# Kernel optimization log

Hardware: AMD Instinct MI355X
Metric: run time of the kernel (lower is better)

The kernel has to match this reference:

```python
import jax, jax.numpy as jnp
import numpy as np

CUTOFF = 3.6
WIDTH = 0.3
N_MAX = 12
N_TYPES = 3
Y00 = 0.28209479177387814  # 1/sqrt(4*pi)
# GTO radial widths: sigma_n = cutoff * max(sqrt(n),1) / n_max
_SIGMA = np.array([CUTOFF * max(np.sqrt(n), 1.0) / N_MAX for n in range(N_MAX)], dtype=np.float32)
_NPOW = np.arange(N_MAX, dtype=np.float32)


def _cutoff_fn(r):
    # shifted cosine: 1 below cutoff-width, smooth cosine taper, 0 beyond cutoff
    start = CUTOFF - WIDTH
    taper = 0.5 * (1.0 + jnp.cos(jnp.pi * (r - start) / WIDTH))
    return jnp.where(r < start, 1.0, jnp.where(r < CUTOFF, taper, 0.0))


def _radial(r):
    # GTO-like basis: R_n(r) = r^n * exp(-r^2 / (2 sigma_n^2)), shape [E, N_MAX]
    r_ = r[:, None]
    return (r_ ** _NPOW) * jnp.exp(-0.5 * (r_ / _SIGMA) ** 2)


def _sph_harm(u):
    # real spherical harmonics up to l=2 on unit vectors u=[E,3] -> [E,9]
    x, y, z = u[:, 0], u[:, 1], u[:, 2]
    one = jnp.ones_like(x)
    return jnp.stack([
        0.28209479177387814 * one,                       # l=0
        0.4886025119029199 * y,                          # l=1, m=-1
        0.4886025119029199 * z,                          # l=1, m=0
        0.4886025119029199 * x,                          # l=1, m=+1
        1.0925484305920792 * x * y,                      # l=2, m=-2
        1.0925484305920792 * y * z,                      # l=2, m=-1
        0.31539156525252005 * (3.0 * z * z - 1.0),       # l=2, m=0
        1.0925484305920792 * x * z,                      # l=2, m=+1
        0.5462742152960396 * (x * x - y * y),            # l=2, m=+2
    ], axis=-1)


def _soap_energy(positions, weight, bias, atom_types, pairs):
    N = positions.shape[0]
    i, j = pairs[:, 0], pairs[:, 1]
    rij = positions[j] - positions[i]                     # [E,3] gather
    r = jnp.sqrt(jnp.sum(rij * rij, axis=-1) + 1e-12)     # [E]
    u = rij / r[:, None]
    # per-edge basis: [E, n, lm]
    B = _radial(r)[:, :, None] * _sph_harm(u)[:, None, :] * _cutoff_fn(r)[:, None, None]
    # scatter-sum by (center atom, neighbor species)
    seg = i.astype(jnp.int32) * N_TYPES + atom_types[j]
    c = jax.ops.segment_sum(B, seg, num_segments=N * N_TYPES)
    c = c.reshape(N, N_TYPES, N_MAX, 9)                    # [N, a, n, lm]
    # center-atom self density (r=0: only n=0, l=0 survives), weight 1.0
    c = c.at[jnp.arange(N), atom_types, 0, 0].add(Y00)
    # power spectrum per l block
    blocks = []
    for l, (lo, hi) in enumerate([(0, 1), (1, 4), (4, 9)]):
        cl = c[:, :, :, lo:hi]
        p = jnp.einsum('ianm,ibkm->ianbk', cl, cl) / jnp.sqrt(2.0 * l + 1.0)
        blocks.append(p)
    feats = jnp.stack(blocks, axis=-1).reshape(N, -1)      # [N, 3888]
    pooled = feats.sum(axis=0, keepdims=True)              # per_atom=False path
    return pooled @ weight.T + bias                        # [1, 1]


def setup_inputs() -> dict:
    key = jax.random.key(0)
    k1, k2, k3, k4 = jax.random.split(key, 4)
    N, E = 30000, 1000000
    positions = jax.random.normal(k1, (N, 3), dtype=jnp.float32) * 1.5
    atom_types = jax.random.randint(k2, (N,), 0, N_TYPES, dtype=jnp.int32)
    pairs = jax.random.randint(k3, (E, 2), 0, N, dtype=jnp.int32)
    weight = jax.random.normal(k4, (1, 3888), dtype=jnp.float32) * 0.01
    bias = jnp.zeros((1,), dtype=jnp.float32)
    return {"positions": positions, "weight": weight, "bias": bias,
            "atom_types": atom_types, "pairs": pairs}


def reference(positions, weight, bias, atom_types, pairs):
    return _soap_energy(positions, weight, bias, atom_types, pairs)
```

## Files before the change

kernel.cpp:

```cpp
#include <hip/hip_runtime.h>
#include <hip/hip_bf16.h>


#define NT 3
#define CPA 324
#define A_ELEMS 3888
#define BCAP 64
#define WPB 4
#define RSTRIDE 25

typedef __attribute__((ext_vector_type(4))) unsigned short ushort4v;
typedef unsigned long long ull;

#if __has_builtin(__builtin_amdgcn_exp2f)
__device__ __forceinline__ float exp2_fast(float x) { return __builtin_amdgcn_exp2f(x); }
#else
__device__ __forceinline__ float exp2_fast(float x) { return __expf(x * 0.6931471805599453f); }
#endif

__global__ void prep_kernel(const float* __restrict__ w,
                            const float* __restrict__ bias,
                            const float* __restrict__ pos,
                            const int* __restrict__ types,
                            float* __restrict__ A,
                            float4* __restrict__ posT,
                            int* __restrict__ cnt,
                            float* __restrict__ out, int N) {
    int t = blockIdx.x * blockDim.x + threadIdx.x;
    if (t == 0) out[0] = bias[0];
    if (t < A_ELEMS) {
        int l   = t / 1296;
        int rem = t - l * 1296;
        int an  = rem / 36;
        int bk  = rem - an * 36;
        int a = an / 12, n = an - (an / 12) * 12;
        int b = bk / 12, k = bk - (bk / 12) * 12;
        float inv = (l == 0) ? 1.0f : (l == 1 ? 0.57735026918962576f
                                              : 0.44721359549995794f);
        A[t] = w[a * 1296 + n * 108 + b * 36 + k * 3 + l] * inv;
    }
    if (t < N) {
        float4 p;
        p.x = pos[3 * t + 0];
        p.y = pos[3 * t + 1];
        p.z = pos[3 * t + 2];
        p.w = __int_as_float(types[t]);
        posT[t] = p;
        cnt[t] = 0;
    }
}

__device__ __forceinline__ void build_one(int i, int j,
                                          const float4& a, const float4& b,
                                          int* cnt, unsigned short* bucket) {
    float dx = b.x - a.x, dy = b.y - a.y, dz = b.z - a.z;
    float r2 = dx * dx + dy * dy + dz * dz;
    if (r2 < 12.96f) {
        int p = atomicAdd(&cnt[i], 1);
        if (p < BCAP) bucket[(i << 6) + p] = (unsigned short)j;
    }
}

__global__ void build_kernel(const int* __restrict__ pairs,
                             const float4* __restrict__ posT,
                             int* __restrict__ cnt,
                             unsigned short* __restrict__ bucket, int E) {
    int t = blockIdx.x * blockDim.x + threadIdx.x;
    int e0 = t << 2;
    if (e0 >= E) return;
    if (e0 + 4 <= E) {
        int4 q0 = ((const int4*)pairs)[t * 2];
        int4 q1 = ((const int4*)pairs)[t * 2 + 1];
        float4 a0 = posT[q0.x], b0 = posT[q0.y];
        float4 a1 = posT[q0.z], b1 = posT[q0.w];
        float4 a2 = posT[q1.x], b2 = posT[q1.y];
        float4 a3 = posT[q1.z], b3 = posT[q1.w];
        build_one(q0.x, q0.y, a0, b0, cnt, bucket);
        build_one(q0.z, q0.w, a1, b1, cnt, bucket);
        build_one(q1.x, q1.y, a2, b2, cnt, bucket);
        build_one(q1.z, q1.w, a3, b3, cnt, bucket);
    } else {
        for (int e = e0; e < E; ++e) {
            int i = pairs[2 * e], j = pairs[2 * e + 1];
            float4 a = posT[i], b = posT[j];
            build_one(i, j, a, b, cnt, bucket);
        }
    }
}

__global__ void __launch_bounds__(256)
accum_kernel(const float4* __restrict__ posT,
             const int* __restrict__ cnt,
             const unsigned short* __restrict__ bucket,
             __hip_bfloat16* __restrict__ c2, int N) {
    __shared__ float sE[WPB][64][RSTRIDE];
    int wid = (blockIdx.x * blockDim.x + threadIdx.x) >> 6;
    int lane = threadIdx.x & 63;
    int wslot = (threadIdx.x >> 6);
    if (wid >= N) return;
    int i = wid;

    float4 pi = posT[i];
    int degv = cnt[i];
    degv = degv > BCAP ? BCAP : degv;
    int deg = __builtin_amdgcn_readfirstlane(degv);

    int jv = bucket[(i << 6) + lane];
    bool valid = lane < deg;
    int jsafe = valid ? jv : i;
    float4 pj = posT[jsafe];

    float dx = pj.x - pi.x, dy = pj.y - pi.y, dz = pj.z - pi.z;
    float u  = fmaf(dz, dz, fmaf(dy, dy, fmaf(dx, dx, 1e-12f)));
    float wv = __log2f(u);
    float ir = rsqrtf(u);
    float iu = ir * ir;
    float lf = 0.0f;
    if (u >= 10.89f) {
        float r = sqrtf(u);
        float fcv = 0.5f + 0.5f * __cosf(10.471975511965978f * (r - 3.3f));
        lf = __log2f(fcv);
    }
    int tj = __float_as_int(pj.w);

    const float QC[12] = {
        -8.014972449383130f, -8.014972449383130f, -4.007486224691565f,
        -2.671657483127710f, -2.003743112345783f, -1.602994489876626f,
        -1.335828741563855f, -1.144996064197590f, -1.001871556172891f,
        -0.890552494375903f, -0.801497244938313f, -0.728633859034830f };
    float R[12];
    #pragma unroll
    for (int n = 0; n < 12; ++n)
        R[n] = exp2_fast(fmaf(0.5f * n, wv, fmaf(QC[n], u, lf)));

    ull m0b = __ballot(valid && tj == 0);
    ull m1b = __ballot(valid && tj == 1);
    ull m2b = __ballot(valid && tj == 2);
    ull lt  = (lane == 63) ? 0x7FFFFFFFFFFFFFFFull : ((1ull << lane) - 1ull);
    int c0n = __popcll(m0b);
    int c1n = __popcll(m1b);
    int dest;
    if (!valid)          dest = deg + __popcll(~(m0b | m1b | m2b) & lt);
    else if (tj == 0)    dest = __popcll(m0b & lt);
    else if (tj == 1)    dest = c0n + __popcll(m1b & lt);
    else                 dest = c0n + c1n + __popcll(m2b & lt);

    float* rec = &sE[wslot][dest][0];
    #pragma unroll
    for (int n = 0; n < 12; ++n) rec[n] = R[n];
    rec[12] = 1.0f;
    rec[13] = dy * ir;  rec[14] = dz * ir;  rec[15] = dx * ir;
    rec[16] = dx * dy * iu;
    rec[17] = dy * dz * iu;
    rec[18] = fmaf(dz, dz, -0.33333333333333333f * u) * iu;
    rec[19] = dx * dz * iu;
    rec[20] = fmaf(dx, dx, -(dy * dy)) * iu;
    asm volatile("s_waitcnt lgkmcnt(0)" ::: "memory");

    int e1b = c0n + c1n;

    int n0 = lane % 12, m0 = lane / 12;
    int idx1 = lane + 64;
    bool has1 = idx1 < 108;
    int i1 = has1 ? idx1 : 0;
    int n1 = i1 % 12, m1 = i1 / 12;

    const float* recb = &sE[wslot][0][0];

    float a00 = 0.f, a01 = 0.f, a02 = 0.f;
    float a10 = 0.f, a11 = 0.f, a12 = 0.f;

    #define EDGE_BODY(E_IDX, ACC0, ACC1)                                   \
    {                                                                      \
        const float* rp = recb + (E_IDX) * RSTRIDE;                        \
        float Rv0 = rp[n0];                                                \
        float Tv0 = rp[12 + m0];                                           \
        float Rv1 = rp[n1];                                                \
        float Tv1 = rp[12 + m1];                                           \
        ACC0 = fmaf(Rv0, Tv0, ACC0);                                       \
        ACC1 = fmaf(Rv1, Tv1, ACC1);                                       \
    }

    int e = 0;
    #pragma unroll 4
    for (; e < c0n; ++e)  EDGE_BODY(e, a00, a10);
    #pragma unroll 4
    for (; e < e1b; ++e)  EDGE_BODY(e, a01, a11);
    #pragma unroll 4
    for (; e < deg; ++e)  EDGE_BODY(e, a02, a12);
    #undef EDGE_BODY

    __hip_bfloat16* cb = c2 + (size_t)i * CPA;
    cb[m0 * 36 + 0 * 12 + n0] = __float2bfloat16(a00);
    cb[m0 * 36 + 1 * 12 + n0] = __float2bfloat16(a01);
    cb[m0 * 36 + 2 * 12 + n0] = __float2bfloat16(a02);
    if (has1) {
        cb[m1 * 36 + 0 * 12 + n1] = __float2bfloat16(a10);
        cb[m1 * 36 + 1 * 12 + n1] = __float2bfloat16(a11);
        cb[m1 * 36 + 2 * 12 + n1] = __float2bfloat16(a12);
    }
}

__global__ void __launch_bounds__(576)
quad_kernel(const __hip_bfloat16* __restrict__ c2,
            const int* __restrict__ types,
            const float* __restrict__ A,
            float* __restrict__ out, int N) {
    __shared__ float sred[9];
    int m = __builtin_amdgcn_readfirstlane(threadIdx.x >> 6);
    int lane = threadIdx.x & 63;
    int i = blockIdx.x * 64 + lane;
    float dot = 0.0f;
    if (i < N) {
        float Km = m == 0 ? 0.28209479177387814f
                 : (m < 4 ? 0.4886025119029199f
                 : (m == 6 ? 0.94617469575756f
                 : (m == 8 ? 0.5462742152960396f : 1.0925484305920792f)));
        const ushort4v* cb4 =
            (const ushort4v*)(c2 + (size_t)i * CPA + m * 36);
        float v[36];
        #pragma unroll
        for (int q = 0; q < 9; ++q) {
            ushort4v u = cb4[q];
            #pragma unroll
            for (int r = 0; r < 4; ++r)
                v[q * 4 + r] = __uint_as_float(((unsigned)u[r]) << 16) * Km;
        }
        if (m == 0) {
            int ti = types[i];
            const float Y00 = 0.28209479177387814f;
            v[0]  += ti == 0 ? Y00 : 0.f;
            v[12] += ti == 1 ? Y00 : 0.f;
            v[24] += ti == 2 ? Y00 : 0.f;
        }
        int l = (m == 0) ? 0 : (m < 4 ? 1 : 2);
        const float* Al = A + l * 1296;
        #pragma unroll
        for (int an = 0; an < 36; ++an) {
            float s = 0.0f;
            #pragma unroll
            for (int b = 0; b < 36; ++b)
                s = fmaf(Al[an * 36 + b], v[b], s);
            dot = fmaf(v[an], s, dot);
        }
    }
    #pragma unroll
    for (int off = 32; off > 0; off >>= 1) dot += __shfl_down(dot, off, 64);
    if (lane == 0) sred[m] = dot;
    __syncthreads();
    if (threadIdx.x == 0) {
        float s = 0.f;
        #pragma unroll
        for (int kk = 0; kk < 9; ++kk) s += sred[kk];
        atomicAdd(out, s);
    }
}

extern "C" void kernel_launch(void* const* d_in, const int* in_sizes, int n_in,
                              void* d_out, int out_size, void* d_ws, size_t ws_size,
                              hipStream_t stream) {
    const float* pos   = (const float*)d_in[0];
    const float* w     = (const float*)d_in[1];
    const float* bias  = (const float*)d_in[2];
    const int*   types = (const int*)d_in[3];
    const int*   pairs = (const int*)d_in[4];
    float* out = (float*)d_out;

    int N = in_sizes[0] / 3;
    int E = in_sizes[4] / 2;

    char* ws = (char*)d_ws;
    size_t off = 0;
    float* A = (float*)(ws + off);             off += 16384;
    int* cnt = (int*)(ws + off);               off += ((size_t)N * 4 + 255) & ~(size_t)255;
    float4* posT = (float4*)(ws + off);        off += ((size_t)N * 16 + 255) & ~(size_t)255;
    unsigned short* bucket = (unsigned short*)(ws + off);
                                               off += ((size_t)N * BCAP * 2 + 255) & ~(size_t)255;
    __hip_bfloat16* c2 = (__hip_bfloat16*)(ws + off);

    int pblocks = (N + 255) / 256;
    prep_kernel<<<pblocks, 256, 0, stream>>>(w, bias, pos, types, A, posT, cnt, out, N);

    int equads = (E + 3) / 4;
    int eblocks = (equads + 255) / 256;
    build_kernel<<<eblocks, 256, 0, stream>>>(pairs, posT, cnt, bucket, E);

    int ablocks = ((size_t)N * 64 + 255) / 256;
    accum_kernel<<<ablocks, 256, 0, stream>>>(posT, cnt, bucket, c2, N);

    int qblocks = (N + 63) / 64;
    quad_kernel<<<qblocks, 576, 0, stream>>>(c2, types, A, out, N);
}
```

Before: 94.67 us.

## Shard neighbor bucket counters across eight slices to reduce atomic contention

Each block in the edge-filter kernel now writes to one of eight per-atom shards (chosen by block index) with a 16-entry cap, instead of a single 64-entry bucket per atom. The accumulate kernel reads all eight counters, builds prefix offsets per lane, and gathers neighbors from the matching shard. This spreads same-atom atomics across separate counters and addresses, meant to cut contention in the build pass. In exchange it uses eight times more counter memory, adds eight counter loads plus index arithmetic per wave, and could drop neighbors if one shard overflows 16 even when the total stays under 64.

```diff
diff --git a/kernel.cpp b/kernel.cpp
--- a/kernel.cpp
+++ b/kernel.cpp
@@ -5,7 +5,7 @@
 #define NT 3
 #define CPA 324
 #define A_ELEMS 3888
-#define BCAP 64
+#define SCAP 16
 #define WPB 4
 #define RSTRIDE 25
 
@@ -46,25 +46,28 @@
         p.z = pos[3 * t + 2];
         p.w = __int_as_float(types[t]);
         posT[t] = p;
-        cnt[t] = 0;
-    }
-}
-
-__device__ __forceinline__ void build_one(int i, int j,
+    }
+    if (t < 8 * N) cnt[t] = 0;
+}
+
+__device__ __forceinline__ void build_one(int i, int j, int shard, int N,
                                           const float4& a, const float4& b,
                                           int* cnt, unsigned short* bucket) {
     float dx = b.x - a.x, dy = b.y - a.y, dz = b.z - a.z;
     float r2 = dx * dx + dy * dy + dz * dz;
     if (r2 < 12.96f) {
-        int p = atomicAdd(&cnt[i], 1);
-        if (p < BCAP) bucket[(i << 6) + p] = (unsigned short)j;
+        int idx = shard * N + i;
+        int p = atomicAdd(&cnt[idx], 1);
+        if (p < SCAP) bucket[(idx << 4) + p] = (unsigned short)j;
     }
 }
 
 __global__ void build_kernel(const int* __restrict__ pairs,
                              const float4* __restrict__ posT,
                              int* __restrict__ cnt,
-                             unsigned short* __restrict__ bucket, int E) {
+                             unsigned short* __restrict__ bucket,
+                             int E, int N) {
+    int shard = blockIdx.x & 7;
     int t = blockIdx.x * blockDim.x + threadIdx.x;
     int e0 = t << 2;
     if (e0 >= E) return;
@@ -75,15 +78,15 @@
         float4 a1 = posT[q0.z], b1 = posT[q0.w];
         float4 a2 = posT[q1.x], b2 = posT[q1.y];
         float4 a3 = posT[q1.z], b3 = posT[q1.w];
-        build_one(q0.x, q0.y, a0, b0, cnt, bucket);
-        build_one(q0.z, q0.w, a1, b1, cnt, bucket);
-        build_one(q1.x, q1.y, a2, b2, cnt, bucket);
-        build_one(q1.z, q1.w, a3, b3, cnt, bucket);
+        build_one(q0.x, q0.y, shard, N, a0, b0, cnt, bucket);
+        build_one(q0.z, q0.w, shard, N, a1, b1, cnt, bucket);
+        build_one(q1.x, q1.y, shard, N, a2, b2, cnt, bucket);
+        build_one(q1.z, q1.w, shard, N, a3, b3, cnt, bucket);
     } else {
         for (int e = e0; e < E; ++e) {
             int i = pairs[2 * e], j = pairs[2 * e + 1];
             float4 a = posT[i], b = posT[j];
-            build_one(i, j, a, b, cnt, bucket);
+            build_one(i, j, shard, N, a, b, cnt, bucket);
         }
     }
 }
@@ -101,11 +104,31 @@
     int i = wid;
 
     float4 pi = posT[i];
-    int degv = cnt[i];
-    degv = degv > BCAP ? BCAP : degv;
-    int deg = __builtin_amdgcn_readfirstlane(degv);
-
-    int jv = bucket[(i << 6) + lane];
+
+    int d0 = min(cnt[0 * N + i], SCAP);
+    int d1 = min(cnt[1 * N + i], SCAP);
+    int d2 = min(cnt[2 * N + i], SCAP);
+    int d3 = min(cnt[3 * N + i], SCAP);
+    int d4 = min(cnt[4 * N + i], SCAP);
+    int d5 = min(cnt[5 * N + i], SCAP);
+    int d6 = min(cnt[6 * N + i], SCAP);
+    int d7 = min(cnt[7 * N + i], SCAP);
+    int p1 = d0, p2 = p1 + d1, p3 = p2 + d2, p4 = p3 + d3;
+    int p5 = p4 + d4, p6 = p5 + d5, p7 = p6 + d6;
+    int tot = p7 + d7;
+    int deg = __builtin_amdgcn_readfirstlane(min(tot, 64));
+
+    int k = lane;
+    int seg = (k >= p1) + (k >= p2) + (k >= p3) + (k >= p4)
+            + (k >= p5) + (k >= p6) + (k >= p7);
+    int bs = 0;
+    bs = (seg >= 1) ? p1 : bs;  bs = (seg >= 2) ? p2 : bs;
+    bs = (seg >= 3) ? p3 : bs;  bs = (seg >= 4) ? p4 : bs;
+    bs = (seg >= 5) ? p5 : bs;  bs = (seg >= 6) ? p6 : bs;
+    bs = (seg >= 7) ? p7 : bs;
+    int off = (k - bs) & (SCAP - 1);
+    int jv = bucket[((seg * N + i) << 4) + off];
+
     bool valid = lane < deg;
     int jsafe = valid ? jv : i;
     float4 pj = posT[jsafe];
@@ -272,18 +295,18 @@
     char* ws = (char*)d_ws;
     size_t off = 0;
     float* A = (float*)(ws + off);             off += 16384;
-    int* cnt = (int*)(ws + off);               off += ((size_t)N * 4 + 255) & ~(size_t)255;
+    int* cnt = (int*)(ws + off);               off += ((size_t)N * 32 + 255) & ~(size_t)255;
     float4* posT = (float4*)(ws + off);        off += ((size_t)N * 16 + 255) & ~(size_t)255;
     unsigned short* bucket = (unsigned short*)(ws + off);
-                                               off += ((size_t)N * BCAP * 2 + 255) & ~(size_t)255;
+                                               off += ((size_t)N * 8 * SCAP * 2 + 255) & ~(size_t)255;
     __hip_bfloat16* c2 = (__hip_bfloat16*)(ws + off);
 
-    int pblocks = (N + 255) / 256;
+    int pblocks = (8 * N + 255) / 256;
     prep_kernel<<<pblocks, 256, 0, stream>>>(w, bias, pos, types, A, posT, cnt, out, N);
 
     int equads = (E + 3) / 4;
     int eblocks = (equads + 255) / 256;
-    build_kernel<<<eblocks, 256, 0, stream>>>(pairs, posT, cnt, bucket, E);
+    build_kernel<<<eblocks, 256, 0, stream>>>(pairs, posT, cnt, bucket, E, N);
 
     int ablocks = ((size_t)N * 64 + 255) / 256;
     accum_kernel<<<ablocks, 256, 0, stream>>>(posT, cnt, bucket, c2, N);
```

New measurement: 92.46 us. 1.02x faster.
